# Performance work log

Measured on AMD Instinct MI355X. Metric: run time of the kernel, lower is better.

Reference implementation:

```python
import jax, jax.numpy as jnp
import numpy as np

N, E, NNZ, R, F = 100000, 100000, 800000, 4, 64

def setup_inputs() -> dict:
    key = jax.random.key(0)
    k1, k2, k3, k4, k5 = jax.random.split(key, 5)
    x = jax.random.normal(k1, (N, F), dtype=jnp.float32)
    rank_masks = jax.random.uniform(k2, (R, E), dtype=jnp.float32)
    vals = jnp.ones((NNZ,), dtype=jnp.float32)
    he_idxs = jax.random.randint(k3, (E,), 0, E, dtype=jnp.int64)
    rows = jax.random.randint(k4, (NNZ,), 0, N, dtype=jnp.int64)
    cols = jax.random.randint(k5, (NNZ,), 0, E, dtype=jnp.int64)
    return {"x": x, "rank_masks": rank_masks, "vals": vals,
            "he_idxs": he_idxs, "rows": rows, "cols": cols}

def reference(x, rank_masks, vals, he_idxs, rows, cols):
    # incidence: sparse [N, E] in COO form (rows=node idx, cols=hyperedge idx, vals)
    n, f = x.shape
    r = rank_masks.shape[0]
    e = he_idxs.shape[0]
    # hyperedge_features = incidence^T @ x  -> [E, F]  (gather nodes, scatter to hyperedges)
    he_feat = jax.ops.segment_sum(x[rows] * vals[:, None], cols, num_segments=e)
    # rank_masks[:, he_idxs] -> [R, E]; einsum('ij,jk->jik') -> [E, R, F]
    rm = rank_masks[:, he_idxs]
    ranks_features = rm.T[:, :, None] * he_feat[:, None, :]          # [E, R, F]
    flat = ranks_features.reshape(e, r * f)                          # [E, R*F]
    # sequences = incidence @ flat -> [N, R*F]
    seq = jax.ops.segment_sum(flat[cols] * vals[:, None], rows, num_segments=n)
    seq = seq.reshape(n, r, f)
    # last rank slot is the node's own features
    seq = seq.at[:, -1, :].set(x)
    return seq
```

## Files before the change

### kernel.cpp

```cpp
#include <hip/hip_runtime.h>

static constexpr int F   = 64;
static constexpr int RF  = 256;
static constexpr int CAP = 48;

__device__ inline float bf2f(unsigned int u16) {
    return __uint_as_float(u16 << 16);
}
__device__ inline unsigned short f2bf(float f) {
    unsigned int x = __float_as_uint(f);
    return (unsigned short)((x + 0x7fffu + ((x >> 16) & 1u)) >> 16);
}
__device__ inline float4 bf4_to_f4(uint2 u) {
    float4 r;
    r.x = bf2f(u.x & 0xffffu);
    r.y = bf2f(u.x >> 16);
    r.z = bf2f(u.y & 0xffffu);
    r.w = bf2f(u.y >> 16);
    return r;
}
__device__ inline uint2 f4_to_bf4(float4 f) {
    uint2 u;
    u.x = (unsigned int)f2bf(f.x) | ((unsigned int)f2bf(f.y) << 16);
    u.y = (unsigned int)f2bf(f.z) | ((unsigned int)f2bf(f.w) << 16);
    return u;
}


__global__ void k_prep(const int* __restrict__ he_idxs, const float* __restrict__ rm,
                       const float* __restrict__ x,
                       float4* __restrict__ wv, uint2* __restrict__ x_bf,
                       int E, int Nn)
{
    int t = blockIdx.x * 256 + threadIdx.x;
    if (t < E) {
        int idx = he_idxs[t];
        float4 w;
        w.x = rm[idx];
        w.y = rm[(size_t)E + idx];
        w.z = rm[2 * (size_t)E + idx];
        w.w = 0.f;
        wv[t] = w;
    }
    if (t < Nn * 16) {
        float4 v = ((const float4*)x)[t];
        x_bf[t] = f4_to_bf4(v);
    }
}

__global__ void k_scatter_col(const int* __restrict__ rows, const int* __restrict__ cols,
                              const float* __restrict__ vals,
                              int* __restrict__ cur_col, int2* __restrict__ col_pay,
                              int nnz, int E)
{
    int t = blockIdx.x * 256 + threadIdx.x;
    if (t >= nnz) return;
    int c = cols[t];
    int j = atomicAdd(&cur_col[c], 1);
    if (j < CAP)
        col_pay[(size_t)j * E + c] = make_int2(rows[t], __float_as_int(vals[t]));
}

__global__ void k_scatter_row(const int* __restrict__ rows, const int* __restrict__ cols,
                              const float* __restrict__ vals,
                              int* __restrict__ cur_row, int2* __restrict__ row_pay,
                              int nnz, int Nn)
{
    int t = blockIdx.x * 256 + threadIdx.x;
    if (t >= nnz) return;
    int r = rows[t];
    int j = atomicAdd(&cur_row[r], 1);
    if (j < CAP)
        row_pay[(size_t)j * Nn + r] = make_int2(__float_as_int(vals[t]), cols[t]);
}

__device__ inline float4 group_reduce4(float4 a)
{
    a.x += __shfl_xor(a.x, 16); a.y += __shfl_xor(a.y, 16);
    a.z += __shfl_xor(a.z, 16); a.w += __shfl_xor(a.w, 16);
    a.x += __shfl_xor(a.x, 32); a.y += __shfl_xor(a.y, 32);
    a.z += __shfl_xor(a.z, 32); a.w += __shfl_xor(a.w, 32);
    return a;
}

__global__ void k_hefeat(const uint2* __restrict__ x_bf,
                         const int* __restrict__ cur_col,
                         const int2* __restrict__ col_pay,
                         uint2* __restrict__ he_bf, int E)
{
    int wave = threadIdx.x >> 6, lane = threadIdx.x & 63;
    int g = lane >> 4, li = lane & 15;
    int e = blockIdx.x * 4 + wave;
    if (e >= E) return;
    int cnt = min(cur_col[e], CAP);
    float4 acc = make_float4(0.f, 0.f, 0.f, 0.f);
    for (int j = g; j < cnt; j += 4) {
        int2 cp = col_pay[(size_t)j * E + e];
        float v = __int_as_float(cp.y);
        float4 xv = bf4_to_f4(x_bf[(size_t)cp.x * 16 + li]);
        acc.x += v * xv.x; acc.y += v * xv.y;
        acc.z += v * xv.z; acc.w += v * xv.w;
    }
    acc = group_reduce4(acc);
    if (g == 0)
        he_bf[(size_t)e * 16 + li] = f4_to_bf4(acc);
}

__global__ void k_seq(const int* __restrict__ cur_row,
                      const int2* __restrict__ row_pay,
                      const float4* __restrict__ wv,
                      const uint2* __restrict__ he_bf,
                      const float* __restrict__ x,
                      float* __restrict__ out, int Nn)
{
    int wave = threadIdx.x >> 6, lane = threadIdx.x & 63;
    int g = lane >> 4, li = lane & 15;
    int n = blockIdx.x * 4 + wave;
    if (n >= Nn) return;
    int cnt = min(cur_row[n], CAP);
    float4 a0 = make_float4(0.f, 0.f, 0.f, 0.f);
    float4 a1 = a0, a2 = a0;
    for (int j = g; j < cnt; j += 4) {
        int2 rp = row_pay[(size_t)j * Nn + n];
        float v = __int_as_float(rp.x);
        int e = rp.y;
        float4 w = wv[e];
        float4 h = bf4_to_f4(he_bf[(size_t)e * 16 + li]);
        float s0 = w.x * v, s1 = w.y * v, s2 = w.z * v;
        a0.x += s0 * h.x; a0.y += s0 * h.y; a0.z += s0 * h.z; a0.w += s0 * h.w;
        a1.x += s1 * h.x; a1.y += s1 * h.y; a1.z += s1 * h.z; a1.w += s1 * h.w;
        a2.x += s2 * h.x; a2.y += s2 * h.y; a2.z += s2 * h.z; a2.w += s2 * h.w;
    }
    a0 = group_reduce4(a0);
    a1 = group_reduce4(a1);
    a2 = group_reduce4(a2);
    if (g == 0) {
        float4* o = (float4*)(out + (size_t)n * RF);
        o[li]      = a0;
        o[16 + li] = a1;
        o[32 + li] = a2;
        o[48 + li] = ((const float4*)(x + (size_t)n * F))[li];
    }
}

__global__ void k_hefeat_atomic(const float* __restrict__ x,
                                const float* __restrict__ vals,
                                const int* __restrict__ rows,
                                const int* __restrict__ cols,
                                float* __restrict__ out, int nnz)
{
    int t = blockIdx.x * 256 + threadIdx.x;
    int k = t >> 6;
    if (k >= nnz) return;
    int f = t & 63;
    atomicAdd(out + (size_t)cols[k] * RF + 3 * F + f,
              x[(size_t)rows[k] * F + f] * vals[k]);
}

__global__ void k_seq_atomic(const float* __restrict__ rank_masks,
                             const float* __restrict__ vals,
                             const int* __restrict__ he_idxs,
                             const int* __restrict__ rows,
                             const int* __restrict__ cols,
                             float* __restrict__ out, int nnz, int E)
{
    int t = blockIdx.x * 256 + threadIdx.x;
    int k = t >> 6;
    if (k >= nnz) return;
    int f = t & 63;
    int n = rows[k], e = cols[k];
    float v = vals[k];
    int idx = he_idxs[e];
    float hf = out[(size_t)e * RF + 3 * F + f] * v;
    float* base = out + (size_t)n * RF + f;
    atomicAdd(base + 0 * F, rank_masks[idx] * hf);
    atomicAdd(base + 1 * F, rank_masks[(size_t)E + idx] * hf);
    atomicAdd(base + 2 * F, rank_masks[2 * (size_t)E + idx] * hf);
}

__global__ void k_lastrank(const float* __restrict__ x,
                           float* __restrict__ out, int n_nodes)
{
    int t = blockIdx.x * 256 + threadIdx.x;
    if (t >= n_nodes * 16) return;
    int n = t >> 4, li = t & 15;
    ((float4*)(out + (size_t)n * RF + 3 * F))[li] =
        ((const float4*)(x + (size_t)n * F))[li];
}


extern "C" void kernel_launch(void* const* d_in, const int* in_sizes, int n_in,
                              void* d_out, int out_size, void* d_ws, size_t ws_size,
                              hipStream_t stream)
{
    const float* x       = (const float*)d_in[0];
    const float* rm      = (const float*)d_in[1];
    const float* vals    = (const float*)d_in[2];
    const int*   he_idxs = (const int*)d_in[3];
    const int*   rows    = (const int*)d_in[4];
    const int*   cols    = (const int*)d_in[5];
    float* out = (float*)d_out;

    const int nnz = in_sizes[2];
    const int E   = in_sizes[3];
    const int nN  = in_sizes[0] / F;

    const int nnz_blocks  = (nnz + 255) / 256;
    const int seg_blocks  = (E + 3) / 4;
    const int node_blocks = (nN + 3) / 4;
    const int prep_blocks = ((nN * 16 > E ? nN * 16 : E) + 255) / 256;

    {
        char* p = (char*)d_ws;
        uint2* he_bf   = (uint2*)p;  p += (size_t)E * 16 * sizeof(uint2);
        uint2* x_bf    = (uint2*)p;  p += (size_t)nN * 16 * sizeof(uint2);
        int2*  row_pay = (int2*)p;   p += (size_t)CAP * nN * sizeof(int2);
        int2*  col_pay = (int2*)p;   p += (size_t)CAP * E * sizeof(int2);
        float4* wv     = (float4*)p; p += (size_t)E * sizeof(float4);
        int*   cur_row = (int*)p;    p += (size_t)nN * sizeof(int);
        int*   cur_col = (int*)p;    p += (size_t)E * sizeof(int);
        size_t need_fixed = (size_t)(p - (char*)d_ws);

        if (ws_size >= need_fixed) {
            hipMemsetAsync(cur_row, 0, ((size_t)nN + E) * sizeof(int), stream);
            k_prep<<<prep_blocks, 256, 0, stream>>>(he_idxs, rm, x, wv, x_bf, E, nN);
            k_scatter_col<<<nnz_blocks, 256, 0, stream>>>(rows, cols, vals,
                                                          cur_col, col_pay, nnz, E);
            k_scatter_row<<<nnz_blocks, 256, 0, stream>>>(rows, cols, vals,
                                                          cur_row, row_pay, nnz, nN);
            k_hefeat<<<seg_blocks, 256, 0, stream>>>(x_bf, cur_col, col_pay, he_bf, E);
            k_seq<<<node_blocks, 256, 0, stream>>>(cur_row, row_pay, wv, he_bf,
                                                   x, out, nN);
            return;
        }
    }

    hipMemsetAsync(d_out, 0, (size_t)out_size * sizeof(float), stream);
    const int b64 = (nnz * 64 + 255) / 256;
    const int lr_blocks = (nN * 16 + 255) / 256;
    k_hefeat_atomic<<<b64, 256, 0, stream>>>(x, vals, rows, cols, out, nnz);
    k_seq_atomic<<<b64, 256, 0, stream>>>(rm, vals, he_idxs, rows, cols, out, nnz, E);
    k_lastrank<<<lr_blocks, 256, 0, stream>>>(x, out, nN);
}
```

Measured before the change: 205.5 us.

## Merge independent stages into block-partitioned kernels to cut launches

Combines the column scatter, x-to-bf16 conversion and rank-weight gather into one launch partitioned by block index. It also combines the row scatter with the hyperedge feature reduction, which do not depend on each other. The copy of x into the last rank slot moves from the final kernel into the conversion blocks. This removes two kernel launches and their serialization gaps and lets independent work run concurrently. In exchange, the mixed launches may be imbalanced across their block ranges.

```diff
diff --git a/kernel.cpp b/kernel.cpp
--- a/kernel.cpp
+++ b/kernel.cpp
@@ -27,13 +27,33 @@
 }
 
 
-__global__ void k_prep(const int* __restrict__ he_idxs, const float* __restrict__ rm,
-                       const float* __restrict__ x,
-                       float4* __restrict__ wv, uint2* __restrict__ x_bf,
-                       int E, int Nn)
-{
-    int t = blockIdx.x * 256 + threadIdx.x;
-    if (t < E) {
+__global__ void k_phase1(const int* __restrict__ rows, const int* __restrict__ cols,
+                         const float* __restrict__ vals,
+                         const int* __restrict__ he_idxs, const float* __restrict__ rm,
+                         const float* __restrict__ x,
+                         int* __restrict__ cur_col, int2* __restrict__ col_pay,
+                         float4* __restrict__ wv, uint2* __restrict__ x_bf,
+                         float* __restrict__ out,
+                         int nnz, int E, int Nn, int scat_blocks, int conv_blocks)
+{
+    int b = blockIdx.x;
+    if (b < scat_blocks) {
+        int t = b * 256 + threadIdx.x;
+        if (t >= nnz) return;
+        int c = cols[t];
+        int j = atomicAdd(&cur_col[c], 1);
+        if (j < CAP)
+            col_pay[(size_t)j * E + c] = make_int2(rows[t], __float_as_int(vals[t]));
+    } else if (b < scat_blocks + conv_blocks) {
+        int t = (b - scat_blocks) * 256 + threadIdx.x;
+        if (t >= Nn * 16) return;
+        float4 v = ((const float4*)x)[t];
+        x_bf[t] = f4_to_bf4(v);
+        int n = t >> 4, li = t & 15;
+        ((float4*)(out + (size_t)n * RF + 3 * F))[li] = v;
+    } else {
+        int t = (b - scat_blocks - conv_blocks) * 256 + threadIdx.x;
+        if (t >= E) return;
         int idx = he_idxs[t];
         float4 w;
         w.x = rm[idx];
@@ -42,36 +62,6 @@
         w.w = 0.f;
         wv[t] = w;
     }
-    if (t < Nn * 16) {
-        float4 v = ((const float4*)x)[t];
-        x_bf[t] = f4_to_bf4(v);
-    }
-}
-
-__global__ void k_scatter_col(const int* __restrict__ rows, const int* __restrict__ cols,
-                              const float* __restrict__ vals,
-                              int* __restrict__ cur_col, int2* __restrict__ col_pay,
-                              int nnz, int E)
-{
-    int t = blockIdx.x * 256 + threadIdx.x;
-    if (t >= nnz) return;
-    int c = cols[t];
-    int j = atomicAdd(&cur_col[c], 1);
-    if (j < CAP)
-        col_pay[(size_t)j * E + c] = make_int2(rows[t], __float_as_int(vals[t]));
-}
-
-__global__ void k_scatter_row(const int* __restrict__ rows, const int* __restrict__ cols,
-                              const float* __restrict__ vals,
-                              int* __restrict__ cur_row, int2* __restrict__ row_pay,
-                              int nnz, int Nn)
-{
-    int t = blockIdx.x * 256 + threadIdx.x;
-    if (t >= nnz) return;
-    int r = rows[t];
-    int j = atomicAdd(&cur_row[r], 1);
-    if (j < CAP)
-        row_pay[(size_t)j * Nn + r] = make_int2(__float_as_int(vals[t]), cols[t]);
 }
 
 __device__ inline float4 group_reduce4(float4 a)
@@ -83,35 +73,47 @@
     return a;
 }
 
-__global__ void k_hefeat(const uint2* __restrict__ x_bf,
-                         const int* __restrict__ cur_col,
-                         const int2* __restrict__ col_pay,
-                         uint2* __restrict__ he_bf, int E)
-{
-    int wave = threadIdx.x >> 6, lane = threadIdx.x & 63;
-    int g = lane >> 4, li = lane & 15;
-    int e = blockIdx.x * 4 + wave;
-    if (e >= E) return;
-    int cnt = min(cur_col[e], CAP);
-    float4 acc = make_float4(0.f, 0.f, 0.f, 0.f);
-    for (int j = g; j < cnt; j += 4) {
-        int2 cp = col_pay[(size_t)j * E + e];
-        float v = __int_as_float(cp.y);
-        float4 xv = bf4_to_f4(x_bf[(size_t)cp.x * 16 + li]);
-        acc.x += v * xv.x; acc.y += v * xv.y;
-        acc.z += v * xv.z; acc.w += v * xv.w;
-    }
-    acc = group_reduce4(acc);
-    if (g == 0)
-        he_bf[(size_t)e * 16 + li] = f4_to_bf4(acc);
-}
-
-__global__ void k_seq(const int* __restrict__ cur_row,
-                      const int2* __restrict__ row_pay,
-                      const float4* __restrict__ wv,
-                      const uint2* __restrict__ he_bf,
-                      const float* __restrict__ x,
-                      float* __restrict__ out, int Nn)
+__global__ void k_phase2(const int* __restrict__ rows, const int* __restrict__ cols,
+                         const float* __restrict__ vals,
+                         const uint2* __restrict__ x_bf,
+                         int* __restrict__ cur_row, int2* __restrict__ row_pay,
+                         const int* __restrict__ cur_col, const int2* __restrict__ col_pay,
+                         uint2* __restrict__ he_bf,
+                         int nnz, int E, int Nn, int scat_blocks)
+{
+    int b = blockIdx.x;
+    if (b < scat_blocks) {
+        int t = b * 256 + threadIdx.x;
+        if (t >= nnz) return;
+        int r = rows[t];
+        int j = atomicAdd(&cur_row[r], 1);
+        if (j < CAP)
+            row_pay[(size_t)j * Nn + r] = make_int2(__float_as_int(vals[t]), cols[t]);
+    } else {
+        int wave = threadIdx.x >> 6, lane = threadIdx.x & 63;
+        int g = lane >> 4, li = lane & 15;
+        int e = (b - scat_blocks) * 4 + wave;
+        if (e >= E) return;
+        int cnt = min(cur_col[e], CAP);
+        float4 acc = make_float4(0.f, 0.f, 0.f, 0.f);
+        for (int j = g; j < cnt; j += 4) {
+            int2 cp = col_pay[(size_t)j * E + e];
+            float v = __int_as_float(cp.y);
+            float4 xv = bf4_to_f4(x_bf[(size_t)cp.x * 16 + li]);
+            acc.x += v * xv.x; acc.y += v * xv.y;
+            acc.z += v * xv.z; acc.w += v * xv.w;
+        }
+        acc = group_reduce4(acc);
+        if (g == 0)
+            he_bf[(size_t)e * 16 + li] = f4_to_bf4(acc);
+    }
+}
+
+__global__ void k_seq3(const int* __restrict__ cur_row,
+                       const int2* __restrict__ row_pay,
+                       const float4* __restrict__ wv,
+                       const uint2* __restrict__ he_bf,
+                       float* __restrict__ out, int Nn)
 {
     int wave = threadIdx.x >> 6, lane = threadIdx.x & 63;
     int g = lane >> 4, li = lane & 15;
@@ -139,7 +141,6 @@
         o[li]      = a0;
         o[16 + li] = a1;
         o[32 + li] = a2;
-        o[48 + li] = ((const float4*)(x + (size_t)n * F))[li];
     }
 }
 
@@ -205,10 +206,11 @@
     const int E   = in_sizes[3];
     const int nN  = in_sizes[0] / F;
 
-    const int nnz_blocks  = (nnz + 255) / 256;
+    const int scat_blocks = (nnz + 255) / 256;
+    const int conv_blocks = (nN * 16 + 255) / 256;
+    const int wv_blocks   = (E + 255) / 256;
     const int seg_blocks  = (E + 3) / 4;
     const int node_blocks = (nN + 3) / 4;
-    const int prep_blocks = ((nN * 16 > E ? nN * 16 : E) + 255) / 256;
 
     {
         char* p = (char*)d_ws;
@@ -223,14 +225,16 @@
 
         if (ws_size >= need_fixed) {
             hipMemsetAsync(cur_row, 0, ((size_t)nN + E) * sizeof(int), stream);
-            k_prep<<<prep_blocks, 256, 0, stream>>>(he_idxs, rm, x, wv, x_bf, E, nN);
-            k_scatter_col<<<nnz_blocks, 256, 0, stream>>>(rows, cols, vals,
-                                                          cur_col, col_pay, nnz, E);
-            k_scatter_row<<<nnz_blocks, 256, 0, stream>>>(rows, cols, vals,
-                                                          cur_row, row_pay, nnz, nN);
-            k_hefeat<<<seg_blocks, 256, 0, stream>>>(x_bf, cur_col, col_pay, he_bf, E);
-            k_seq<<<node_blocks, 256, 0, stream>>>(cur_row, row_pay, wv, he_bf,
-                                                   x, out, nN);
+            k_phase1<<<scat_blocks + conv_blocks + wv_blocks, 256, 0, stream>>>(
+                rows, cols, vals, he_idxs, rm, x,
+                cur_col, col_pay, wv, x_bf, out,
+                nnz, E, nN, scat_blocks, conv_blocks);
+            k_phase2<<<scat_blocks + seg_blocks, 256, 0, stream>>>(
+                rows, cols, vals, x_bf,
+                cur_row, row_pay, cur_col, col_pay, he_bf,
+                nnz, E, nN, scat_blocks);
+            k_seq3<<<node_blocks, 256, 0, stream>>>(cur_row, row_pay, wv, he_bf,
+                                                    out, nN);
             return;
         }
     }
```

Result: faster. 195.0 us (-5.1%).

## Pad atomic counters, unroll gather loops by two, move x copy into prep kernel

Applied to the files above, without the earlier changes.

The row and column atomic counters are spaced 8 ints apart (cshift=3) to cut same-cache-line contention during the scatter atomics, with a fallback to dense counters when the workspace is too small. The hefeat and seq gather loops now process two payload entries per iteration, which adds memory-level parallelism. The last-rank copy of x into the output moves from k_seq into the prep/convert kernel, so k_seq writes only three rank slices. The padded counters cost a larger memset and a bigger counter footprint.

```diff
diff --git a/kernel.cpp b/kernel.cpp
--- a/kernel.cpp
+++ b/kernel.cpp
@@ -27,13 +27,23 @@
 }
 
 
-__global__ void k_prep(const int* __restrict__ he_idxs, const float* __restrict__ rm,
-                       const float* __restrict__ x,
-                       float4* __restrict__ wv, uint2* __restrict__ x_bf,
-                       int E, int Nn)
-{
-    int t = blockIdx.x * 256 + threadIdx.x;
-    if (t < E) {
+__global__ void k_conv_wv(const float* __restrict__ x,
+                          const int* __restrict__ he_idxs, const float* __restrict__ rm,
+                          uint2* __restrict__ x_bf, float* __restrict__ out,
+                          float4* __restrict__ wv,
+                          int E, int Nn, int conv_blocks)
+{
+    int b = blockIdx.x;
+    if (b < conv_blocks) {
+        int t = b * 256 + threadIdx.x;
+        if (t >= Nn * 16) return;
+        float4 v = ((const float4*)x)[t];
+        x_bf[t] = f4_to_bf4(v);
+        int n = t >> 4, li = t & 15;
+        ((float4*)(out + (size_t)n * RF + 3 * F))[li] = v;
+    } else {
+        int t = (b - conv_blocks) * 256 + threadIdx.x;
+        if (t >= E) return;
         int idx = he_idxs[t];
         float4 w;
         w.x = rm[idx];
@@ -42,21 +52,17 @@
         w.w = 0.f;
         wv[t] = w;
     }
-    if (t < Nn * 16) {
-        float4 v = ((const float4*)x)[t];
-        x_bf[t] = f4_to_bf4(v);
-    }
 }
 
 __global__ void k_scatter_col(const int* __restrict__ rows, const int* __restrict__ cols,
                               const float* __restrict__ vals,
                               int* __restrict__ cur_col, int2* __restrict__ col_pay,
-                              int nnz, int E)
+                              int nnz, int E, int cshift)
 {
     int t = blockIdx.x * 256 + threadIdx.x;
     if (t >= nnz) return;
     int c = cols[t];
-    int j = atomicAdd(&cur_col[c], 1);
+    int j = atomicAdd(&cur_col[c << cshift], 1);
     if (j < CAP)
         col_pay[(size_t)j * E + c] = make_int2(rows[t], __float_as_int(vals[t]));
 }
@@ -64,12 +70,12 @@
 __global__ void k_scatter_row(const int* __restrict__ rows, const int* __restrict__ cols,
                               const float* __restrict__ vals,
                               int* __restrict__ cur_row, int2* __restrict__ row_pay,
-                              int nnz, int Nn)
+                              int nnz, int Nn, int cshift)
 {
     int t = blockIdx.x * 256 + threadIdx.x;
     if (t >= nnz) return;
     int r = rows[t];
-    int j = atomicAdd(&cur_row[r], 1);
+    int j = atomicAdd(&cur_row[r << cshift], 1);
     if (j < CAP)
         row_pay[(size_t)j * Nn + r] = make_int2(__float_as_int(vals[t]), cols[t]);
 }
@@ -86,50 +92,70 @@
 __global__ void k_hefeat(const uint2* __restrict__ x_bf,
                          const int* __restrict__ cur_col,
                          const int2* __restrict__ col_pay,
-                         uint2* __restrict__ he_bf, int E)
+                         uint2* __restrict__ he_bf, int E, int cshift)
 {
     int wave = threadIdx.x >> 6, lane = threadIdx.x & 63;
     int g = lane >> 4, li = lane & 15;
     int e = blockIdx.x * 4 + wave;
     if (e >= E) return;
-    int cnt = min(cur_col[e], CAP);
+    int cnt = min(cur_col[e << cshift], CAP);
     float4 acc = make_float4(0.f, 0.f, 0.f, 0.f);
-    for (int j = g; j < cnt; j += 4) {
-        int2 cp = col_pay[(size_t)j * E + e];
-        float v = __int_as_float(cp.y);
-        float4 xv = bf4_to_f4(x_bf[(size_t)cp.x * 16 + li]);
-        acc.x += v * xv.x; acc.y += v * xv.y;
-        acc.z += v * xv.z; acc.w += v * xv.w;
+    for (int j = g; j < cnt; j += 8) {
+        int2 cp0 = col_pay[(size_t)j * E + e];
+        bool has1 = (j + 4) < cnt;
+        int2 cp1 = has1 ? col_pay[(size_t)(j + 4) * E + e] : make_int2(0, 0);
+        float v0 = __int_as_float(cp0.y);
+        float4 x0 = bf4_to_f4(x_bf[(size_t)cp0.x * 16 + li]);
+        if (has1) {
+            float v1 = __int_as_float(cp1.y);
+            float4 x1 = bf4_to_f4(x_bf[(size_t)cp1.x * 16 + li]);
+            acc.x += v1 * x1.x; acc.y += v1 * x1.y;
+            acc.z += v1 * x1.z; acc.w += v1 * x1.w;
+        }
+        acc.x += v0 * x0.x; acc.y += v0 * x0.y;
+        acc.z += v0 * x0.z; acc.w += v0 * x0.w;
     }
     acc = group_reduce4(acc);
     if (g == 0)
         he_bf[(size_t)e * 16 + li] = f4_to_bf4(acc);
 }
 
-__global__ void k_seq(const int* __restrict__ cur_row,
-                      const int2* __restrict__ row_pay,
-                      const float4* __restrict__ wv,
-                      const uint2* __restrict__ he_bf,
-                      const float* __restrict__ x,
-                      float* __restrict__ out, int Nn)
+__global__ void k_seq3(const int* __restrict__ cur_row,
+                       const int2* __restrict__ row_pay,
+                       const float4* __restrict__ wv,
+                       const uint2* __restrict__ he_bf,
+                       float* __restrict__ out, int Nn, int cshift)
 {
     int wave = threadIdx.x >> 6, lane = threadIdx.x & 63;
     int g = lane >> 4, li = lane & 15;
     int n = blockIdx.x * 4 + wave;
     if (n >= Nn) return;
-    int cnt = min(cur_row[n], CAP);
+    int cnt = min(cur_row[n << cshift], CAP);
     float4 a0 = make_float4(0.f, 0.f, 0.f, 0.f);
     float4 a1 = a0, a2 = a0;
-    for (int j = g; j < cnt; j += 4) {
-        int2 rp = row_pay[(size_t)j * Nn + n];
-        float v = __int_as_float(rp.x);
-        int e = rp.y;
-        float4 w = wv[e];
-        float4 h = bf4_to_f4(he_bf[(size_t)e * 16 + li]);
-        float s0 = w.x * v, s1 = w.y * v, s2 = w.z * v;
-        a0.x += s0 * h.x; a0.y += s0 * h.y; a0.z += s0 * h.z; a0.w += s0 * h.w;
-        a1.x += s1 * h.x; a1.y += s1 * h.y; a1.z += s1 * h.z; a1.w += s1 * h.w;
-        a2.x += s2 * h.x; a2.y += s2 * h.y; a2.z += s2 * h.z; a2.w += s2 * h.w;
+    for (int j = g; j < cnt; j += 8) {
+        int2 rp0 = row_pay[(size_t)j * Nn + n];
+        bool has1 = (j + 4) < cnt;
+        int2 rp1 = has1 ? row_pay[(size_t)(j + 4) * Nn + n] : make_int2(0, 0);
+
+        float v0 = __int_as_float(rp0.x);
+        int e0 = rp0.y;
+        float4 w0 = wv[e0];
+        float4 h0 = bf4_to_f4(he_bf[(size_t)e0 * 16 + li]);
+        if (has1) {
+            float v1 = __int_as_float(rp1.x);
+            int e1 = rp1.y;
+            float4 w1 = wv[e1];
+            float4 h1 = bf4_to_f4(he_bf[(size_t)e1 * 16 + li]);
+            float t0 = w1.x * v1, t1 = w1.y * v1, t2 = w1.z * v1;
+            a0.x += t0 * h1.x; a0.y += t0 * h1.y; a0.z += t0 * h1.z; a0.w += t0 * h1.w;
+            a1.x += t1 * h1.x; a1.y += t1 * h1.y; a1.z += t1 * h1.z; a1.w += t1 * h1.w;
+            a2.x += t2 * h1.x; a2.y += t2 * h1.y; a2.z += t2 * h1.z; a2.w += t2 * h1.w;
+        }
+        float s0 = w0.x * v0, s1 = w0.y * v0, s2 = w0.z * v0;
+        a0.x += s0 * h0.x; a0.y += s0 * h0.y; a0.z += s0 * h0.z; a0.w += s0 * h0.w;
+        a1.x += s1 * h0.x; a1.y += s1 * h0.y; a1.z += s1 * h0.z; a1.w += s1 * h0.w;
+        a2.x += s2 * h0.x; a2.y += s2 * h0.y; a2.z += s2 * h0.z; a2.w += s2 * h0.w;
     }
     a0 = group_reduce4(a0);
     a1 = group_reduce4(a1);
@@ -139,7 +165,6 @@
         o[li]      = a0;
         o[16 + li] = a1;
         o[32 + li] = a2;
-        o[48 + li] = ((const float4*)(x + (size_t)n * F))[li];
     }
 }
 
@@ -206,31 +231,38 @@
     const int nN  = in_sizes[0] / F;
 
     const int nnz_blocks  = (nnz + 255) / 256;
+    const int conv_blocks = (nN * 16 + 255) / 256;
+    const int wv_blocks   = (E + 255) / 256;
     const int seg_blocks  = (E + 3) / 4;
     const int node_blocks = (nN + 3) / 4;
-    const int prep_blocks = ((nN * 16 > E ? nN * 16 : E) + 255) / 256;
-
-    {
+
+    for (int attempt = 0; attempt < 2; ++attempt) {
+        const int cshift = (attempt == 0) ? 3 : 0;
         char* p = (char*)d_ws;
         uint2* he_bf   = (uint2*)p;  p += (size_t)E * 16 * sizeof(uint2);
         uint2* x_bf    = (uint2*)p;  p += (size_t)nN * 16 * sizeof(uint2);
         int2*  row_pay = (int2*)p;   p += (size_t)CAP * nN * sizeof(int2);
         int2*  col_pay = (int2*)p;   p += (size_t)CAP * E * sizeof(int2);
         float4* wv     = (float4*)p; p += (size_t)E * sizeof(float4);
-        int*   cur_row = (int*)p;    p += (size_t)nN * sizeof(int);
-        int*   cur_col = (int*)p;    p += (size_t)E * sizeof(int);
+        int*   cur_row = (int*)p;    p += ((size_t)nN << cshift) * sizeof(int);
+        int*   cur_col = (int*)p;    p += ((size_t)E << cshift) * sizeof(int);
         size_t need_fixed = (size_t)(p - (char*)d_ws);
 
         if (ws_size >= need_fixed) {
-            hipMemsetAsync(cur_row, 0, ((size_t)nN + E) * sizeof(int), stream);
-            k_prep<<<prep_blocks, 256, 0, stream>>>(he_idxs, rm, x, wv, x_bf, E, nN);
+            hipMemsetAsync(cur_row, 0,
+                           (((size_t)nN + E) << cshift) * sizeof(int), stream);
+            k_conv_wv<<<conv_blocks + wv_blocks, 256, 0, stream>>>(
+                x, he_idxs, rm, x_bf, out, wv, E, nN, conv_blocks);
             k_scatter_col<<<nnz_blocks, 256, 0, stream>>>(rows, cols, vals,
-                                                          cur_col, col_pay, nnz, E);
+                                                          cur_col, col_pay,
+                                                          nnz, E, cshift);
             k_scatter_row<<<nnz_blocks, 256, 0, stream>>>(rows, cols, vals,
-                                                          cur_row, row_pay, nnz, nN);
-            k_hefeat<<<seg_blocks, 256, 0, stream>>>(x_bf, cur_col, col_pay, he_bf, E);
-            k_seq<<<node_blocks, 256, 0, stream>>>(cur_row, row_pay, wv, he_bf,
-                                                   x, out, nN);
+                                                          cur_row, row_pay,
+                                                          nnz, nN, cshift);
+            k_hefeat<<<seg_blocks, 256, 0, stream>>>(x_bf, cur_col, col_pay,
+                                                     he_bf, E, cshift);
+            k_seq3<<<node_blocks, 256, 0, stream>>>(cur_row, row_pay, wv, he_bf,
+                                                    out, nN, cshift);
             return;
         }
     }
```

Measured after the change: 190.7 us. 1.08x faster.
